# Kernel tuning notes

Measured on AMD Instinct MI355X. Metric: run time of the kernel, lower is better.

The kernel has to match this reference:

```python
import jax, jax.numpy as jnp
import numpy as np

B, N, D, H, DM = 4, 1024, 1024, 16, 4096
DH = D // H
SCALE = DH ** -0.5
EPS = 1e-5


def layer_norm(x, g, b):
    mu = jnp.mean(x, axis=-1, keepdims=True)
    var = jnp.mean((x - mu) ** 2, axis=-1, keepdims=True)
    return (x - mu) * jax.lax.rsqrt(var + EPS) * g + b


def mha(q_in, k_in, v_in, Wq, bq, Wk, bk, Wv, bv, Wp, bp):
    # weights stored (in, out); torch Linear equivalent y = x @ W + b
    q = (q_in @ Wq + bq).reshape(B, -1, H, DH).transpose(0, 2, 1, 3)  # (B,H,Nq,DH)
    k = (k_in @ Wk + bk).reshape(B, -1, H, DH).transpose(0, 2, 1, 3)
    v = (v_in @ Wv + bv).reshape(B, -1, H, DH).transpose(0, 2, 1, 3)
    attn = jax.nn.softmax(jnp.einsum('bhqd,bhkd->bhqk', q, k) * SCALE, axis=-1)
    x = jnp.einsum('bhqk,bhkd->bhqd', attn, v).transpose(0, 2, 1, 3).reshape(B, -1, D)
    return x @ Wp + bp


def setup_inputs() -> dict:
    key = jax.random.key(0)
    ks = jax.random.split(key, 32)
    s = 0.02
    inp = {
        'tokens_enc': jax.random.normal(ks[0], (B, N, D), jnp.float32),
        'tokens_dec': jax.random.normal(ks[1], (B, N, D), jnp.float32),
        'PE_enc': jax.random.normal(ks[2], (B, N, D), jnp.float32),
        'PE_dec': jax.random.normal(ks[3], (B, N, D), jnp.float32),
    }
    names = ['sa_Wq', 'sa_Wk', 'sa_Wv', 'sa_Wp', 'ca_Wq', 'ca_Wk', 'ca_Wv', 'ca_Wp']
    for i, n in enumerate(names):
        inp[n] = jax.random.normal(ks[4 + i], (D, D), jnp.float32) * s
        inp[n.replace('W', 'b')] = jnp.zeros((D,), jnp.float32)
    inp['mlp_W1'] = jax.random.normal(ks[12], (D, DM), jnp.float32) * s
    inp['mlp_b1'] = jnp.zeros((DM,), jnp.float32)
    inp['mlp_W2'] = jax.random.normal(ks[13], (DM, D), jnp.float32) * s
    inp['mlp_b2'] = jnp.zeros((D,), jnp.float32)
    for i in (1, 2, 3):
        inp[f'ln{i}_g'] = jnp.ones((D,), jnp.float32)
        inp[f'ln{i}_b'] = jnp.zeros((D,), jnp.float32)
    return inp


def reference(tokens_enc, tokens_dec, PE_enc, PE_dec,
              sa_Wq, sa_bq, sa_Wk, sa_bk, sa_Wv, sa_bv, sa_Wp, sa_bp,
              ca_Wq, ca_bq, ca_Wk, ca_bk, ca_Wv, ca_bv, ca_Wp, ca_bp,
              mlp_W1, mlp_b1, mlp_W2, mlp_b2,
              ln1_g, ln1_b, ln2_g, ln2_b, ln3_g, ln3_b):
    # SA (pre-norm): q=k=ln(x)+PE_dec, v=ln(x)
    x2 = layer_norm(tokens_dec, ln1_g, ln1_b)
    qk = x2 + PE_dec
    tokens_dec = tokens_dec + mha(qk, qk, x2, sa_Wq, sa_bq, sa_Wk, sa_bk, sa_Wv, sa_bv, sa_Wp, sa_bp)
    # CA: q=ln(x)+PE_dec, k=enc+PE_enc, v=enc
    x2 = layer_norm(tokens_dec, ln2_g, ln2_b)
    tokens_dec = tokens_dec + mha(x2 + PE_dec, tokens_enc + PE_enc, tokens_enc,
                                  ca_Wq, ca_bq, ca_Wk, ca_bk, ca_Wv, ca_bv, ca_Wp, ca_bp)
    # FFD
    x2 = layer_norm(tokens_dec, ln3_g, ln3_b)
    h = jax.nn.gelu(x2 @ mlp_W1 + mlp_b1, approximate=False)
    return tokens_dec + (h @ mlp_W2 + mlp_b2)
```

## Files before the change

kernel.cpp:

```cpp
#include <hip/hip_runtime.h>
#include <hip/hip_bf16.h>
#include <math.h>

#define B_ 4
#define N_ 1024
#define D_ 1024
#define H_ 16
#define DH_ 64
#define DM_ 4096
#define NT_ (B_*N_)
#define EPS_ 1e-5f
#define SCALE_ 0.125f
#define CEXP_ 0.1803368801111244f

typedef unsigned short u16;
typedef short s16x8 __attribute__((ext_vector_type(8)));
typedef __bf16 y16x8 __attribute__((ext_vector_type(8)));
typedef float f32x4 __attribute__((ext_vector_type(4)));
typedef float f32x16 __attribute__((ext_vector_type(16)));

#define ZERO16 (f32x16){0.f,0.f,0.f,0.f,0.f,0.f,0.f,0.f,0.f,0.f,0.f,0.f,0.f,0.f,0.f,0.f}

__device__ __forceinline__ u16 f2bs(float f) {
  unsigned int u = __builtin_bit_cast(unsigned int, f);
  u += 0x7fffu + ((u >> 16) & 1u);
  return (u16)(u >> 16);
}

static __device__ __forceinline__ f32x4 MFMA(y16x8 a, y16x8 b, f32x4 c) {
  return __builtin_amdgcn_mfma_f32_16x16x32_bf16(a, b, c, 0, 0, 0);
}
static __device__ __forceinline__ f32x16 MFMA32(y16x8 a, y16x8 b, f32x16 c) {
  return __builtin_amdgcn_mfma_f32_32x32x16_bf16(a, b, c, 0, 0, 0);
}

static __device__ __forceinline__ unsigned cvtpk(float a, float b) {
  unsigned r;
  asm("v_cvt_pk_bf16_f32 %0, %1, %2" : "=v"(r) : "v"(a), "v"(b));
  return r;
}

static __device__ __forceinline__ void async16(void* lds, const void* g) {
  __builtin_amdgcn_global_load_lds(
      (const __attribute__((address_space(1))) unsigned int*)g,
      (__attribute__((address_space(3))) unsigned int*)lds, 16, 0, 0);
}

__global__ __launch_bounds__(256) void k_wtrans8(
    const float* __restrict__ s0, const float* __restrict__ s1,
    const float* __restrict__ s2, const float* __restrict__ s3,
    const float* __restrict__ s4, const float* __restrict__ s5,
    const float* __restrict__ s6, const float* __restrict__ s7,
    u16* __restrict__ dst) {
  const float* W = blockIdx.z == 0 ? s0 : blockIdx.z == 1 ? s1 : blockIdx.z == 2 ? s2
                 : blockIdx.z == 3 ? s3 : blockIdx.z == 4 ? s4 : blockIdx.z == 5 ? s5
                 : blockIdx.z == 6 ? s6 : s7;
  u16* Wt = dst + (size_t)blockIdx.z * D_ * D_;
  __shared__ u16 tile[32][33];
  int n0 = blockIdx.x * 32, k0 = blockIdx.y * 32;
  int tx = threadIdx.x & 31, ty = threadIdx.x >> 5;
#pragma unroll
  for (int i = 0; i < 4; ++i) {
    int k = k0 + ty + i * 8;
    tile[ty + i * 8][tx] = f2bs(W[(size_t)k * D_ + n0 + tx]);
  }
  __syncthreads();
#pragma unroll
  for (int i = 0; i < 4; ++i) {
    int n = n0 + ty + i * 8;
    Wt[(size_t)n * D_ + k0 + tx] = tile[tx][ty + i * 8];
  }
}

__global__ __launch_bounds__(256) void k_wtrans(const float* __restrict__ W,
                                                u16* __restrict__ Wt,
                                                int K, int Ncols) {
  __shared__ u16 tile[32][33];
  int n0 = blockIdx.x * 32, k0 = blockIdx.y * 32;
  int tx = threadIdx.x & 31, ty = threadIdx.x >> 5;
#pragma unroll
  for (int i = 0; i < 4; ++i) {
    int k = k0 + ty + i * 8;
    tile[ty + i * 8][tx] = f2bs(W[(size_t)k * Ncols + n0 + tx]);
  }
  __syncthreads();
#pragma unroll
  for (int i = 0; i < 4; ++i) {
    int n = n0 + ty + i * 8;
    Wt[(size_t)n * K + k0 + tx] = tile[tx][ty + i * 8];
  }
}

__global__ __launch_bounds__(256) void k_encprep(const float* __restrict__ enc,
                                                 const float* __restrict__ pe,
                                                 u16* __restrict__ encpe,
                                                 u16* __restrict__ encv) {
  int i = blockIdx.x * 256 + threadIdx.x;
  float4 e = ((const float4*)enc)[i];
  float4 p = ((const float4*)pe)[i];
  union { u16 u[4]; uint2 v; } a, b;
  a.u[0] = f2bs(e.x + p.x); a.u[1] = f2bs(e.y + p.y);
  a.u[2] = f2bs(e.z + p.z); a.u[3] = f2bs(e.w + p.w);
  b.u[0] = f2bs(e.x); b.u[1] = f2bs(e.y); b.u[2] = f2bs(e.z); b.u[3] = f2bs(e.w);
  ((uint2*)encpe)[i] = a.v;
  ((uint2*)encv)[i] = b.v;
}

__global__ __launch_bounds__(256) void k_ln(const float* __restrict__ x,
                                            const float* __restrict__ g,
                                            const float* __restrict__ bta,
                                            const float* __restrict__ pe,
                                            u16* __restrict__ x2o,
                                            u16* __restrict__ qko) {
  int row = blockIdx.x;
  int t = threadIdx.x;
  float4 v = ((const float4*)(x + (size_t)row * D_))[t];
  float s = v.x + v.y + v.z + v.w;
#pragma unroll
  for (int o = 1; o < 64; o <<= 1) s += __shfl_xor(s, o, 64);
  __shared__ float red[8];
  if ((t & 63) == 0) red[t >> 6] = s;
  __syncthreads();
  float mean = (red[0] + red[1] + red[2] + red[3]) * (1.0f / D_);
  float dx = v.x - mean, dy = v.y - mean, dz = v.z - mean, dw = v.w - mean;
  float s2 = dx * dx + dy * dy + dz * dz + dw * dw;
#pragma unroll
  for (int o = 1; o < 64; o <<= 1) s2 += __shfl_xor(s2, o, 64);
  if ((t & 63) == 0) red[4 + (t >> 6)] = s2;
  __syncthreads();
  float var = (red[4] + red[5] + red[6] + red[7]) * (1.0f / D_);
  float rstd = rsqrtf(var + EPS_);
  float4 gv = ((const float4*)g)[t];
  float4 bv = ((const float4*)bta)[t];
  float y0 = dx * rstd * gv.x + bv.x;
  float y1 = dy * rstd * gv.y + bv.y;
  float y2 = dz * rstd * gv.z + bv.z;
  float y3 = dw * rstd * gv.w + bv.w;
  union { u16 u[4]; uint2 v2; } o1;
  o1.u[0] = f2bs(y0); o1.u[1] = f2bs(y1); o1.u[2] = f2bs(y2); o1.u[3] = f2bs(y3);
  ((uint2*)(x2o + (size_t)row * D_))[t] = o1.v2;
  if (pe) {
    float4 pv = ((const float4*)(pe + (size_t)row * D_))[t];
    union { u16 u[4]; uint2 v2; } o2;
    o2.u[0] = f2bs(y0 + pv.x); o2.u[1] = f2bs(y1 + pv.y);
    o2.u[2] = f2bs(y2 + pv.z); o2.u[3] = f2bs(y3 + pv.w);
    ((uint2*)(qko + (size_t)row * D_))[t] = o2.v2;
  }
}

template <int EPI, int BM>
__global__ __launch_bounds__(512) void k_gemm(const u16* __restrict__ A,
                                              const u16* __restrict__ Bt,
                                              const float* __restrict__ bias,
                                              const float* __restrict__ res,
                                              float* __restrict__ outf,
                                              u16* __restrict__ outb,
                                              int M, int Nn, int K, int ldo) {
  constexpr int BN = 128, BK = 64;
  constexpr int FM = BM / 32;
  __shared__ __align__(128) char smem[2][(BM + BN) * BK * 2];
  const int t = threadIdx.x;
  const int wave = t >> 6, lane = t & 63, lg = lane >> 4, lc = lane & 15;
  const int nwg = gridDim.x * gridDim.y;
  const int bid = blockIdx.y * gridDim.x + blockIdx.x;
  const int lb = (bid & 7) * (nwg >> 3) + (bid >> 3);
  const int bx = lb % gridDim.x, by = lb / gridDim.x;
  const int m0 = by * BM, n0 = bx * BN;
  const int wm = (wave >> 2) * (BM / 2), wn = (wave & 3) * 32;
  f32x4 acc[FM][2];
#pragma unroll
  for (int i = 0; i < FM; ++i)
#pragma unroll
    for (int j = 0; j < 2; ++j) acc[i][j] = (f32x4){0.f, 0.f, 0.f, 0.f};
  const char* Ag = (const char*)(A + (size_t)m0 * K);
  const char* Bg = (const char*)(Bt + (size_t)n0 * K);
  const int sr = t >> 3, sp = t & 7;

  auto stage = [&](int bufi, int kt) {
    char* sA = smem[bufi];
    char* sB = smem[bufi] + BM * BK * 2;
#pragma unroll
    for (int rr = 0; rr < BM / 64; ++rr) {
      int row = rr * 64 + sr;
      int c = sp ^ (row & 7);
      async16(sA + (size_t)row * 128 + sp * 16,
              Ag + ((size_t)row * K + kt + c * 8) * 2);
    }
#pragma unroll
    for (int rr = 0; rr < 2; ++rr) {
      int row = rr * 64 + sr;
      int c = sp ^ (row & 7);
      async16(sB + (size_t)row * 128 + sp * 16,
              Bg + ((size_t)row * K + kt + c * 8) * 2);
    }
  };
  auto compute = [&](int bufi) {
    const char* sA = smem[bufi];
    const char* sB = smem[bufi] + BM * BK * 2;
#pragma unroll
    for (int ks = 0; ks < 2; ++ks) {
      y16x8 af[FM], bfr[2];
#pragma unroll
      for (int fm = 0; fm < FM; ++fm) {
        int R = wm + fm * 16 + lc;
        int pc = (ks * 4 + lg) ^ (R & 7);
        af[fm] = *(const y16x8*)(sA + (size_t)R * 128 + pc * 16);
      }
#pragma unroll
      for (int fn = 0; fn < 2; ++fn) {
        int R = wn + fn * 16 + lc;
        int pc = (ks * 4 + lg) ^ (R & 7);
        bfr[fn] = *(const y16x8*)(sB + (size_t)R * 128 + pc * 16);
      }
#pragma unroll
      for (int fm = 0; fm < FM; ++fm)
#pragma unroll
        for (int fn = 0; fn < 2; ++fn)
          acc[fm][fn] = MFMA(af[fm], bfr[fn], acc[fm][fn]);
    }
  };

  stage(0, 0);
  __syncthreads();
  int cur = 0;
  for (int kt = BK; kt < K; kt += BK) {
    stage(cur ^ 1, kt);
    compute(cur);
    __syncthreads();
    cur ^= 1;
  }
  compute(cur);

#pragma unroll
  for (int fm = 0; fm < FM; ++fm)
#pragma unroll
    for (int fn = 0; fn < 2; ++fn)
#pragma unroll
      for (int j = 0; j < 4; ++j) {
        int row = m0 + wm + fm * 16 + lg * 4 + j;
        int col = n0 + wn + fn * 16 + lc;
        float vv = acc[fm][fn][j] + bias[col];
        size_t idx = (size_t)row * ldo + col;
        if constexpr (EPI == 0) {
          outb[idx] = f2bs(vv);
        } else if constexpr (EPI == 1) {
          outf[idx] = vv + res[idx];
        } else {
          float gx = 0.5f * vv * (1.0f + erff(vv * 0.70710678118f));
          outb[idx] = f2bs(gx);
        }
      }
}

__global__ __launch_bounds__(512) void k_gemmG(
    const u16* __restrict__ A0, const u16* __restrict__ A1,
    const u16* __restrict__ A2, const u16* __restrict__ A3,
    const u16* __restrict__ A4, const u16* __restrict__ W0,
    const u16* __restrict__ W1, const u16* __restrict__ W2,
    const u16* __restrict__ W3, const u16* __restrict__ W4,
    const float* __restrict__ b0, const float* __restrict__ b1,
    const float* __restrict__ b2, const float* __restrict__ b3,
    const float* __restrict__ b4, u16* __restrict__ qk1,
    u16* __restrict__ vt1, u16* __restrict__ qk2, u16* __restrict__ vt2) {
  constexpr int BM = 128, BN = 128, BK = 64, K = D_;
  __shared__ __align__(128) char smem[2][(BM + BN) * BK * 2];
  const int z = blockIdx.z;
  const u16* A = z == 0 ? A0 : z == 1 ? A1 : z == 2 ? A2 : z == 3 ? A3 : A4;
  const u16* Bt = z == 0 ? W0 : z == 1 ? W1 : z == 2 ? W2 : z == 3 ? W3 : W4;
  const float* bias = z == 0 ? b0 : z == 1 ? b1 : z == 2 ? b2 : z == 3 ? b3 : b4;
  const int t = threadIdx.x;
  const int wave = t >> 6, lane = t & 63, lg = lane >> 4, lc = lane & 15;
  const int nwg = gridDim.x * gridDim.y;
  const int bid = blockIdx.y * gridDim.x + blockIdx.x;
  const int lb = (bid & 7) * (nwg >> 3) + (bid >> 3);
  const int bx = lb % gridDim.x, by = lb / gridDim.x;
  const int m0 = by * BM, n0 = bx * BN;
  const int wm = (wave >> 2) * 64, wn = (wave & 3) * 32;
  f32x4 acc[4][2];
#pragma unroll
  for (int i = 0; i < 4; ++i)
#pragma unroll
    for (int j = 0; j < 2; ++j) acc[i][j] = (f32x4){0.f, 0.f, 0.f, 0.f};
  const char* Ag = (const char*)(A + (size_t)m0 * K);
  const char* Bg = (const char*)(Bt + (size_t)n0 * K);
  const int sr = t >> 3, sp = t & 7;

  auto stage = [&](int bufi, int kt) {
    char* sA = smem[bufi];
    char* sB = smem[bufi] + BM * BK * 2;
#pragma unroll
    for (int rr = 0; rr < 2; ++rr) {
      int row = rr * 64 + sr;
      int c = sp ^ (row & 7);
      async16(sA + (size_t)row * 128 + sp * 16,
              Ag + ((size_t)row * K + kt + c * 8) * 2);
      async16(sB + (size_t)row * 128 + sp * 16,
              Bg + ((size_t)row * K + kt + c * 8) * 2);
    }
  };
  auto compute = [&](int bufi) {
    const char* sA = smem[bufi];
    const char* sB = smem[bufi] + BM * BK * 2;
#pragma unroll
    for (int ks = 0; ks < 2; ++ks) {
      y16x8 af[4], bfr[2];
#pragma unroll
      for (int fm = 0; fm < 4; ++fm) {
        int R = wm + fm * 16 + lc;
        int pc = (ks * 4 + lg) ^ (R & 7);
        af[fm] = *(const y16x8*)(sA + (size_t)R * 128 + pc * 16);
      }
#pragma unroll
      for (int fn = 0; fn < 2; ++fn) {
        int R = wn + fn * 16 + lc;
        int pc = (ks * 4 + lg) ^ (R & 7);
        bfr[fn] = *(const y16x8*)(sB + (size_t)R * 128 + pc * 16);
      }
#pragma unroll
      for (int fm = 0; fm < 4; ++fm)
#pragma unroll
        for (int fn = 0; fn < 2; ++fn)
          acc[fm][fn] = MFMA(af[fm], bfr[fn], acc[fm][fn]);
    }
  };

  stage(0, 0);
  __syncthreads();
  int cur = 0;
  for (int kt = BK; kt < K; kt += BK) {
    stage(cur ^ 1, kt);
    compute(cur);
    __syncthreads();
    cur ^= 1;
  }
  compute(cur);

  const bool isV = (z == 2) || (z == 4);
  if (!isV) {
    u16* outqk = (z == 3) ? qk2 : qk1;
    const int coff = (z == 1 || z == 3) ? D_ : 0;
#pragma unroll
    for (int fm = 0; fm < 4; ++fm)
#pragma unroll
      for (int fn = 0; fn < 2; ++fn)
#pragma unroll
        for (int j = 0; j < 4; ++j) {
          int row = m0 + wm + fm * 16 + lg * 4 + j;
          int col = n0 + wn + fn * 16 + lc;
          outqk[(size_t)row * (2 * D_) + coff + col] =
              f2bs(acc[fm][fn][j] + bias[col]);
        }
  } else {
    u16* outvt = (z == 2) ? vt1 : vt2;
#pragma unroll
    for (int fm = 0; fm < 4; ++fm)
#pragma unroll
      for (int fn = 0; fn < 2; ++fn) {
        int row0 = m0 + wm + fm * 16 + lg * 4;
        int col = n0 + wn + fn * 16 + lc;
        int bb = row0 >> 10, nn = row0 & (N_ - 1);
        int h = col >> 6, dh = col & 63;
        float bcol = bias[col];
        union { u16 u[4]; uint2 v; } pk;
#pragma unroll
        for (int j = 0; j < 4; ++j) pk.u[j] = f2bs(acc[fm][fn][j] + bcol);
        *(uint2*)&outvt[(((size_t)bb * H_ + h) * DH_ + dh) * N_ + nn] = pk.v;
      }
  }
}

__global__ __launch_bounds__(256) void k_attn(const u16* __restrict__ q, int qs,
                                              const u16* __restrict__ k, int ks2,
                                              const u16* __restrict__ vt,
                                              u16* __restrict__ out) {
  __shared__ __align__(16) u16 Kl[64][64];
  __shared__ __align__(16) u16 Vl[64][64];
  __shared__ __align__(16) u16 Ol[4][32][72];
  const int lb = blockIdx.x;
  const int bh = (lb & 7) | ((lb >> 6) << 3);
  const int qb = (lb >> 3) & 7;
  const int b = bh >> 4, h = bh & 15;
  const int t = threadIdx.x, wave = t >> 6, lane = t & 63;
  const int ql = lane & 31, hi = lane >> 5;
  const int q0 = qb * 128 + wave * 32;
  const u16* qp = q + ((size_t)b * N_ + q0) * qs + h * DH_;
  const u16* kp = k + (size_t)b * N_ * ks2 + h * DH_;
  const u16* vp = vt + ((size_t)bh * DH_) * N_;

  y16x8 aq[4];
#pragma unroll
  for (int s = 0; s < 4; ++s)
    aq[s] = *(const y16x8*)(qp + (size_t)ql * qs + s * 16 + hi * 8);

  f32x16 o0 = ZERO16, o1 = ZERO16;
  float m_r = -1e30f, l_r = 0.f;

  const int srow0 = t >> 3, sc = t & 7;
  s16x8 kreg[2], vreg[2];
#pragma unroll
  for (int rr = 0; rr < 2; ++rr) {
    int row = rr * 32 + srow0;
    kreg[rr] = *(const s16x8*)(kp + (size_t)row * ks2 + sc * 8);
    vreg[rr] = *(const s16x8*)(vp + (size_t)row * N_ + sc * 8);
  }

  for (int kt = 0; kt < N_; kt += 64) {
    __syncthreads();
#pragma unroll
    for (int rr = 0; rr < 2; ++rr) {
      int row = rr * 32 + srow0;
      int pc2 = sc ^ (row & 7);
      *(s16x8*)&Kl[row][pc2 * 8] = kreg[rr];
      *(s16x8*)&Vl[row][pc2 * 8] = vreg[rr];
    }
    __syncthreads();
    if (kt + 64 < N_) {
#pragma unroll
      for (int rr = 0; rr < 2; ++rr) {
        int row = rr * 32 + srow0;
        kreg[rr] = *(const s16x8*)(kp + (size_t)(kt + 64 + row) * ks2 + sc * 8);
        vreg[rr] = *(const s16x8*)(vp + (size_t)row * N_ + kt + 64 + sc * 8);
      }
    }

    f32x16 st0 = ZERO16, st1 = ZERO16;
    __builtin_amdgcn_s_setprio(1);
#pragma unroll
    for (int s = 0; s < 4; ++s) {
      int pc0 = ((s * 2 + hi) ^ (ql & 7)) * 8;
      y16x8 ak0 = *(const y16x8*)&Kl[ql][pc0];
      y16x8 ak1 = *(const y16x8*)&Kl[32 + ql][pc0];
      st0 = MFMA32(ak0, aq[s], st0);
      st1 = MFMA32(ak1, aq[s], st1);
    }
    __builtin_amdgcn_s_setprio(0);

    float mx = st0[0];
#pragma unroll
    for (int r = 1; r < 16; ++r) mx = fmaxf(mx, st0[r]);
#pragma unroll
    for (int r = 0; r < 16; ++r) mx = fmaxf(mx, st1[r]);
    mx = fmaxf(mx, __shfl_xor(mx, 32, 64));
    if (!__all(mx - m_r <= 32.f)) {
      float mn = fmaxf(m_r, mx);
      float corr = exp2f((m_r - mn) * CEXP_);
      l_r *= corr;
      o0 = o0 * corr;
      o1 = o1 * corr;
      m_r = mn;
    }
    float ps = 0.f;
#pragma unroll
    for (int r = 0; r < 16; ++r) {
      float e = exp2f((st0[r] - m_r) * CEXP_); st0[r] = e; ps += e;
    }
#pragma unroll
    for (int r = 0; r < 16; ++r) {
      float e = exp2f((st1[r] - m_r) * CEXP_); st1[r] = e; ps += e;
    }
    ps += __shfl_xor(ps, 32, 64);
    l_r += ps;

    __builtin_amdgcn_s_setprio(1);
#pragma unroll
    for (int ks = 0; ks < 4; ++ks) {
      unsigned A0, A1, B0, B1;
      if (ks < 2) {
        const int il = ks * 8;
        A0 = cvtpk(st0[il + 0], st0[il + 1]);
        A1 = cvtpk(st0[il + 2], st0[il + 3]);
        B0 = cvtpk(st0[il + 4], st0[il + 5]);
        B1 = cvtpk(st0[il + 6], st0[il + 7]);
      } else {
        const int il = (ks - 2) * 8;
        A0 = cvtpk(st1[il + 0], st1[il + 1]);
        A1 = cvtpk(st1[il + 2], st1[il + 3]);
        B0 = cvtpk(st1[il + 4], st1[il + 5]);
        B1 = cvtpk(st1[il + 6], st1[il + 7]);
      }
      asm("v_permlane32_swap_b32 %0, %1" : "+v"(A0), "+v"(B0));
      asm("v_permlane32_swap_b32 %0, %1" : "+v"(A1), "+v"(B1));
      union { unsigned w[4]; y16x8 v; } fr;
      fr.w[0] = A0; fr.w[1] = A1; fr.w[2] = B0; fr.w[3] = B1;
      int pc = ((ks * 2 + hi) ^ (ql & 7)) * 8;
      y16x8 bv0 = *(const y16x8*)&Vl[ql][pc];
      y16x8 bv1 = *(const y16x8*)&Vl[32 + ql][pc];
      o0 = MFMA32(bv0, fr.v, o0);
      o1 = MFMA32(bv1, fr.v, o1);
    }
    __builtin_amdgcn_s_setprio(0);
  }

  float rl = 1.f / l_r;
#pragma unroll
  for (int rq = 0; rq < 4; ++rq)
#pragma unroll
    for (int e = 0; e < 4; e += 2) {
      *(unsigned*)&Ol[wave][ql][8 * rq + 4 * hi + e] =
          cvtpk(o0[rq * 4 + e] * rl, o0[rq * 4 + e + 1] * rl);
      *(unsigned*)&Ol[wave][ql][32 + 8 * rq + 4 * hi + e] =
          cvtpk(o1[rq * 4 + e] * rl, o1[rq * 4 + e + 1] * rl);
    }
#pragma unroll
  for (int pp = 0; pp < 4; ++pp) {
    int row = pp * 8 + (lane >> 3);
    s16x8 vv = *(const s16x8*)&Ol[wave][row][(lane & 7) * 8];
    *(s16x8*)(out + ((size_t)b * N_ + q0 + row) * D_ + h * DH_ + (lane & 7) * 8) = vv;
  }
}

extern "C" void kernel_launch(void* const* d_in, const int* in_sizes, int n_in,
                              void* d_out, int out_size, void* d_ws, size_t ws_size,
                              hipStream_t stream) {
  const float* tokens_enc = (const float*)d_in[0];
  const float* tokens_dec = (const float*)d_in[1];
  const float* PE_enc = (const float*)d_in[2];
  const float* PE_dec = (const float*)d_in[3];
  const float* sa_Wq = (const float*)d_in[4];  const float* sa_bq = (const float*)d_in[5];
  const float* sa_Wk = (const float*)d_in[6];  const float* sa_bk = (const float*)d_in[7];
  const float* sa_Wv = (const float*)d_in[8];  const float* sa_bv = (const float*)d_in[9];
  const float* sa_Wp = (const float*)d_in[10]; const float* sa_bp = (const float*)d_in[11];
  const float* ca_Wq = (const float*)d_in[12]; const float* ca_bq = (const float*)d_in[13];
  const float* ca_Wk = (const float*)d_in[14]; const float* ca_bk = (const float*)d_in[15];
  const float* ca_Wv = (const float*)d_in[16]; const float* ca_bv = (const float*)d_in[17];
  const float* ca_Wp = (const float*)d_in[18]; const float* ca_bp = (const float*)d_in[19];
  const float* mlp_W1 = (const float*)d_in[20]; const float* mlp_b1 = (const float*)d_in[21];
  const float* mlp_W2 = (const float*)d_in[22]; const float* mlp_b2 = (const float*)d_in[23];
  const float* ln1_g = (const float*)d_in[24]; const float* ln1_b = (const float*)d_in[25];
  const float* ln2_g = (const float*)d_in[26]; const float* ln2_b = (const float*)d_in[27];
  const float* ln3_g = (const float*)d_in[28]; const float* ln3_b = (const float*)d_in[29];

  char* wsp = (char*)d_ws;
  size_t off = 0;
  auto alloc = [&](size_t bytes) -> char* {
    char* p = wsp + off;
    off += (bytes + 255) & ~(size_t)255;
    return p;
  };
  u16* w8   = (u16*)alloc((size_t)8 * D_ * D_ * 2);
  u16* w1T  = (u16*)alloc((size_t)DM_ * D_ * 2);
  u16* w2T  = (u16*)alloc((size_t)D_ * DM_ * 2);
  u16* encpe = (u16*)alloc((size_t)NT_ * D_ * 2);
  u16* encv  = (u16*)alloc((size_t)NT_ * D_ * 2);
  u16* x2b = (u16*)alloc((size_t)NT_ * D_ * 2);
  u16* qkb = (u16*)alloc((size_t)NT_ * D_ * 2);
  u16* qkm = (u16*)alloc((size_t)NT_ * 2 * D_ * 2);
  u16* qkm2 = (u16*)alloc((size_t)NT_ * 2 * D_ * 2);
  u16* vtb = (u16*)alloc((size_t)NT_ * D_ * 2);
  u16* vtb2 = (u16*)alloc((size_t)NT_ * D_ * 2);
  u16* attb = (u16*)alloc((size_t)NT_ * D_ * 2);
  float* dec1 = (float*)alloc((size_t)NT_ * D_ * 4);
  float* dec2 = (float*)alloc((size_t)NT_ * D_ * 4);
  u16* hb = (u16*)alloc((size_t)NT_ * DM_ * 2);

  const size_t DD = (size_t)D_ * D_;
  u16* wqT  = w8;
  u16* wkT  = w8 + 1 * DD;
  u16* wvT  = w8 + 2 * DD;
  u16* wpT  = w8 + 3 * DD;
  u16* cwqT = w8 + 4 * DD;
  u16* cwkT = w8 + 5 * DD;
  u16* cwvT = w8 + 6 * DD;
  u16* cwpT = w8 + 7 * DD;

  k_wtrans8<<<dim3(32, 32, 8), 256, 0, stream>>>(sa_Wq, sa_Wk, sa_Wv, sa_Wp,
                                                 ca_Wq, ca_Wk, ca_Wv, ca_Wp, w8);
  k_wtrans<<<dim3(128, 32), 256, 0, stream>>>(mlp_W1, w1T, D_, DM_);
  k_wtrans<<<dim3(32, 128), 256, 0, stream>>>(mlp_W2, w2T, DM_, D_);
  k_encprep<<<dim3(NT_ * D_ / 1024), 256, 0, stream>>>(tokens_enc, PE_enc, encpe, encv);

  k_ln<<<dim3(NT_), 256, 0, stream>>>(tokens_dec, ln1_g, ln1_b, PE_dec, x2b, qkb);
  k_gemmG<<<dim3(8, 32, 5), 512, 0, stream>>>(
      qkb, qkb, x2b, encpe, encv, wqT, wkT, wvT, cwkT, cwvT,
      sa_bq, sa_bk, sa_bv, ca_bk, ca_bv, qkm, vtb, qkm2, vtb2);
  k_attn<<<dim3(512), 256, 0, stream>>>(qkm, 2 * D_, qkm + D_, 2 * D_, vtb, attb);
  k_gemm<1, 64><<<dim3(8, 64), 512, 0, stream>>>(attb, wpT, sa_bp, tokens_dec,
                                                 dec1, nullptr, NT_, D_, D_, D_);

  k_ln<<<dim3(NT_), 256, 0, stream>>>(dec1, ln2_g, ln2_b, PE_dec, x2b, qkb);
  k_gemm<0, 64><<<dim3(8, 64), 512, 0, stream>>>(qkb, cwqT, ca_bq, nullptr,
                                                 nullptr, qkm2, NT_, D_, D_, 2 * D_);
  k_attn<<<dim3(512), 256, 0, stream>>>(qkm2, 2 * D_, qkm2 + D_, 2 * D_, vtb2, attb);
  k_gemm<1, 64><<<dim3(8, 64), 512, 0, stream>>>(attb, cwpT, ca_bp, dec1,
                                                 dec2, nullptr, NT_, D_, D_, D_);

  k_ln<<<dim3(NT_), 256, 0, stream>>>(dec2, ln3_g, ln3_b, nullptr, x2b, nullptr);
  k_gemm<2, 128><<<dim3(32, 32), 512, 0, stream>>>(x2b, w1T, mlp_b1, nullptr,
                                                   nullptr, hb, NT_, DM_, D_, DM_);
  k_gemm<1, 64><<<dim3(8, 64), 512, 0, stream>>>(hb, w2T, mlp_b2, dec2,
                                                 (float*)d_out, nullptr, NT_, D_, DM_, D_);
}
```

Measured before the change: 336.7 us.

## Merge prep kernels, double attention KV tile, shrink MLP1 GEMM tile

Folds the four preprocessing launches (weight transposes and encoder prep) into one kernel that dispatches on block index, which cuts launch overhead. The attention kernel now stages 128 keys per iteration instead of 64 and processes them in two 64-key sub-steps. That halves the barriers and global-load rounds per key, at the cost of more LDS and registers. The first MLP GEMM switches from a 128 to a 64 tile template with twice the grid, trading per-block reuse for more parallelism.

```diff
diff --git a/kernel.cpp b/kernel.cpp
--- a/kernel.cpp
+++ b/kernel.cpp
@@ -46,64 +46,62 @@
       (__attribute__((address_space(3))) unsigned int*)lds, 16, 0, 0);
 }
 
-__global__ __launch_bounds__(256) void k_wtrans8(
+__global__ __launch_bounds__(256) void k_prep(
     const float* __restrict__ s0, const float* __restrict__ s1,
     const float* __restrict__ s2, const float* __restrict__ s3,
     const float* __restrict__ s4, const float* __restrict__ s5,
     const float* __restrict__ s6, const float* __restrict__ s7,
-    u16* __restrict__ dst) {
-  const float* W = blockIdx.z == 0 ? s0 : blockIdx.z == 1 ? s1 : blockIdx.z == 2 ? s2
-                 : blockIdx.z == 3 ? s3 : blockIdx.z == 4 ? s4 : blockIdx.z == 5 ? s5
-                 : blockIdx.z == 6 ? s6 : s7;
-  u16* Wt = dst + (size_t)blockIdx.z * D_ * D_;
+    u16* __restrict__ w8, const float* __restrict__ mW1,
+    u16* __restrict__ w1T, const float* __restrict__ mW2,
+    u16* __restrict__ w2T, const float* __restrict__ enc,
+    const float* __restrict__ pe, u16* __restrict__ encpe,
+    u16* __restrict__ encv) {
   __shared__ u16 tile[32][33];
-  int n0 = blockIdx.x * 32, k0 = blockIdx.y * 32;
-  int tx = threadIdx.x & 31, ty = threadIdx.x >> 5;
-#pragma unroll
-  for (int i = 0; i < 4; ++i) {
-    int k = k0 + ty + i * 8;
-    tile[ty + i * 8][tx] = f2bs(W[(size_t)k * D_ + n0 + tx]);
-  }
-  __syncthreads();
-#pragma unroll
-  for (int i = 0; i < 4; ++i) {
-    int n = n0 + ty + i * 8;
-    Wt[(size_t)n * D_ + k0 + tx] = tile[tx][ty + i * 8];
-  }
-}
-
-__global__ __launch_bounds__(256) void k_wtrans(const float* __restrict__ W,
-                                                u16* __restrict__ Wt,
-                                                int K, int Ncols) {
-  __shared__ u16 tile[32][33];
-  int n0 = blockIdx.x * 32, k0 = blockIdx.y * 32;
-  int tx = threadIdx.x & 31, ty = threadIdx.x >> 5;
-#pragma unroll
-  for (int i = 0; i < 4; ++i) {
-    int k = k0 + ty + i * 8;
-    tile[ty + i * 8][tx] = f2bs(W[(size_t)k * Ncols + n0 + tx]);
-  }
-  __syncthreads();
-#pragma unroll
-  for (int i = 0; i < 4; ++i) {
-    int n = n0 + ty + i * 8;
-    Wt[(size_t)n * K + k0 + tx] = tile[tx][ty + i * 8];
-  }
-}
-
-__global__ __launch_bounds__(256) void k_encprep(const float* __restrict__ enc,
-                                                 const float* __restrict__ pe,
-                                                 u16* __restrict__ encpe,
-                                                 u16* __restrict__ encv) {
-  int i = blockIdx.x * 256 + threadIdx.x;
-  float4 e = ((const float4*)enc)[i];
-  float4 p = ((const float4*)pe)[i];
-  union { u16 u[4]; uint2 v; } a, b;
-  a.u[0] = f2bs(e.x + p.x); a.u[1] = f2bs(e.y + p.y);
-  a.u[2] = f2bs(e.z + p.z); a.u[3] = f2bs(e.w + p.w);
-  b.u[0] = f2bs(e.x); b.u[1] = f2bs(e.y); b.u[2] = f2bs(e.z); b.u[3] = f2bs(e.w);
-  ((uint2*)encpe)[i] = a.v;
-  ((uint2*)encv)[i] = b.v;
+  const int gid = blockIdx.x;
+  const int t = threadIdx.x;
+  if (gid < 16384) {
+    const float* W;
+    u16* Wt;
+    int K, Ncols, n0, k0;
+    if (gid < 8192) {
+      int z = gid >> 10, rem = gid & 1023;
+      W = z == 0 ? s0 : z == 1 ? s1 : z == 2 ? s2 : z == 3 ? s3
+        : z == 4 ? s4 : z == 5 ? s5 : z == 6 ? s6 : s7;
+      Wt = w8 + (size_t)z * D_ * D_;
+      K = D_; Ncols = D_;
+      n0 = (rem & 31) * 32; k0 = (rem >> 5) * 32;
+    } else if (gid < 12288) {
+      int rem = gid - 8192;
+      W = mW1; Wt = w1T; K = D_; Ncols = DM_;
+      n0 = (rem & 127) * 32; k0 = (rem >> 7) * 32;
+    } else {
+      int rem = gid - 12288;
+      W = mW2; Wt = w2T; K = DM_; Ncols = D_;
+      n0 = (rem & 31) * 32; k0 = (rem >> 5) * 32;
+    }
+    int tx = t & 31, ty = t >> 5;
+#pragma unroll
+    for (int i = 0; i < 4; ++i) {
+      int k = k0 + ty + i * 8;
+      tile[ty + i * 8][tx] = f2bs(W[(size_t)k * Ncols + n0 + tx]);
+    }
+    __syncthreads();
+#pragma unroll
+    for (int i = 0; i < 4; ++i) {
+      int n = n0 + ty + i * 8;
+      Wt[(size_t)n * K + k0 + tx] = tile[tx][ty + i * 8];
+    }
+  } else {
+    int i = (gid - 16384) * 256 + t;
+    float4 e = ((const float4*)enc)[i];
+    float4 p = ((const float4*)pe)[i];
+    union { u16 u[4]; uint2 v; } a, b;
+    a.u[0] = f2bs(e.x + p.x); a.u[1] = f2bs(e.y + p.y);
+    a.u[2] = f2bs(e.z + p.z); a.u[3] = f2bs(e.w + p.w);
+    b.u[0] = f2bs(e.x); b.u[1] = f2bs(e.y); b.u[2] = f2bs(e.z); b.u[3] = f2bs(e.w);
+    ((uint2*)encpe)[i] = a.v;
+    ((uint2*)encv)[i] = b.v;
+  }
 }
 
 __global__ __launch_bounds__(256) void k_ln(const float* __restrict__ x,
@@ -373,8 +371,8 @@
                                               const u16* __restrict__ k, int ks2,
                                               const u16* __restrict__ vt,
                                               u16* __restrict__ out) {
-  __shared__ __align__(16) u16 Kl[64][64];
-  __shared__ __align__(16) u16 Vl[64][64];
+  __shared__ __align__(16) u16 Kl[128][64];
+  __shared__ __align__(16) u16 Vl[64][128];
   __shared__ __align__(16) u16 Ol[4][32][72];
   const int lb = blockIdx.x;
   const int bh = (lb & 7) | ((lb >> 6) << 3);
@@ -395,100 +393,103 @@
   f32x16 o0 = ZERO16, o1 = ZERO16;
   float m_r = -1e30f, l_r = 0.f;
 
-  const int srow0 = t >> 3, sc = t & 7;
-  s16x8 kreg[2], vreg[2];
-#pragma unroll
-  for (int rr = 0; rr < 2; ++rr) {
-    int row = rr * 32 + srow0;
-    kreg[rr] = *(const s16x8*)(kp + (size_t)row * ks2 + sc * 8);
-    vreg[rr] = *(const s16x8*)(vp + (size_t)row * N_ + sc * 8);
-  }
-
-  for (int kt = 0; kt < N_; kt += 64) {
+  const int kr = t >> 3, kc = t & 7;
+  const int vr = t >> 4, vc = t & 15;
+  s16x8 kreg[4], vreg[4];
+#pragma unroll
+  for (int rr = 0; rr < 4; ++rr) {
+    kreg[rr] = *(const s16x8*)(kp + (size_t)(rr * 32 + kr) * ks2 + kc * 8);
+    vreg[rr] = *(const s16x8*)(vp + (size_t)(rr * 16 + vr) * N_ + vc * 8);
+  }
+
+  for (int kt = 0; kt < N_; kt += 128) {
     __syncthreads();
 #pragma unroll
-    for (int rr = 0; rr < 2; ++rr) {
-      int row = rr * 32 + srow0;
-      int pc2 = sc ^ (row & 7);
-      *(s16x8*)&Kl[row][pc2 * 8] = kreg[rr];
-      *(s16x8*)&Vl[row][pc2 * 8] = vreg[rr];
+    for (int rr = 0; rr < 4; ++rr) {
+      int krow = rr * 32 + kr;
+      *(s16x8*)&Kl[krow][(kc ^ (krow & 7)) * 8] = kreg[rr];
+      int vrow = rr * 16 + vr;
+      *(s16x8*)&Vl[vrow][(vc ^ (vrow & 15)) * 8] = vreg[rr];
     }
     __syncthreads();
-    if (kt + 64 < N_) {
-#pragma unroll
-      for (int rr = 0; rr < 2; ++rr) {
-        int row = rr * 32 + srow0;
-        kreg[rr] = *(const s16x8*)(kp + (size_t)(kt + 64 + row) * ks2 + sc * 8);
-        vreg[rr] = *(const s16x8*)(vp + (size_t)row * N_ + kt + 64 + sc * 8);
-      }
-    }
-
-    f32x16 st0 = ZERO16, st1 = ZERO16;
-    __builtin_amdgcn_s_setprio(1);
-#pragma unroll
-    for (int s = 0; s < 4; ++s) {
-      int pc0 = ((s * 2 + hi) ^ (ql & 7)) * 8;
-      y16x8 ak0 = *(const y16x8*)&Kl[ql][pc0];
-      y16x8 ak1 = *(const y16x8*)&Kl[32 + ql][pc0];
-      st0 = MFMA32(ak0, aq[s], st0);
-      st1 = MFMA32(ak1, aq[s], st1);
-    }
-    __builtin_amdgcn_s_setprio(0);
-
-    float mx = st0[0];
-#pragma unroll
-    for (int r = 1; r < 16; ++r) mx = fmaxf(mx, st0[r]);
-#pragma unroll
-    for (int r = 0; r < 16; ++r) mx = fmaxf(mx, st1[r]);
-    mx = fmaxf(mx, __shfl_xor(mx, 32, 64));
-    if (!__all(mx - m_r <= 32.f)) {
-      float mn = fmaxf(m_r, mx);
-      float corr = exp2f((m_r - mn) * CEXP_);
-      l_r *= corr;
-      o0 = o0 * corr;
-      o1 = o1 * corr;
-      m_r = mn;
-    }
-    float ps = 0.f;
-#pragma unroll
-    for (int r = 0; r < 16; ++r) {
-      float e = exp2f((st0[r] - m_r) * CEXP_); st0[r] = e; ps += e;
-    }
-#pragma unroll
-    for (int r = 0; r < 16; ++r) {
-      float e = exp2f((st1[r] - m_r) * CEXP_); st1[r] = e; ps += e;
-    }
-    ps += __shfl_xor(ps, 32, 64);
-    l_r += ps;
-
-    __builtin_amdgcn_s_setprio(1);
-#pragma unroll
-    for (int ks = 0; ks < 4; ++ks) {
-      unsigned A0, A1, B0, B1;
-      if (ks < 2) {
-        const int il = ks * 8;
-        A0 = cvtpk(st0[il + 0], st0[il + 1]);
-        A1 = cvtpk(st0[il + 2], st0[il + 3]);
-        B0 = cvtpk(st0[il + 4], st0[il + 5]);
-        B1 = cvtpk(st0[il + 6], st0[il + 7]);
-      } else {
-        const int il = (ks - 2) * 8;
-        A0 = cvtpk(st1[il + 0], st1[il + 1]);
-        A1 = cvtpk(st1[il + 2], st1[il + 3]);
-        B0 = cvtpk(st1[il + 4], st1[il + 5]);
-        B1 = cvtpk(st1[il + 6], st1[il + 7]);
-      }
-      asm("v_permlane32_swap_b32 %0, %1" : "+v"(A0), "+v"(B0));
-      asm("v_permlane32_swap_b32 %0, %1" : "+v"(A1), "+v"(B1));
-      union { unsigned w[4]; y16x8 v; } fr;
-      fr.w[0] = A0; fr.w[1] = A1; fr.w[2] = B0; fr.w[3] = B1;
-      int pc = ((ks * 2 + hi) ^ (ql & 7)) * 8;
-      y16x8 bv0 = *(const y16x8*)&Vl[ql][pc];
-      y16x8 bv1 = *(const y16x8*)&Vl[32 + ql][pc];
-      o0 = MFMA32(bv0, fr.v, o0);
-      o1 = MFMA32(bv1, fr.v, o1);
-    }
-    __builtin_amdgcn_s_setprio(0);
+    if (kt + 128 < N_) {
+#pragma unroll
+      for (int rr = 0; rr < 4; ++rr) {
+        kreg[rr] = *(const s16x8*)(kp + (size_t)(kt + 128 + rr * 32 + kr) * ks2 + kc * 8);
+        vreg[rr] = *(const s16x8*)(vp + (size_t)(rr * 16 + vr) * N_ + kt + 128 + vc * 8);
+      }
+    }
+
+#pragma unroll
+    for (int sub = 0; sub < 2; ++sub) {
+      f32x16 st0 = ZERO16, st1 = ZERO16;
+      __builtin_amdgcn_s_setprio(1);
+#pragma unroll
+      for (int s = 0; s < 4; ++s) {
+        int pc0 = ((s * 2 + hi) ^ (ql & 7)) * 8;
+        y16x8 ak0 = *(const y16x8*)&Kl[sub * 64 + ql][pc0];
+        y16x8 ak1 = *(const y16x8*)&Kl[sub * 64 + 32 + ql][pc0];
+        st0 = MFMA32(ak0, aq[s], st0);
+        st1 = MFMA32(ak1, aq[s], st1);
+      }
+      __builtin_amdgcn_s_setprio(0);
+
+      float mx = st0[0];
+#pragma unroll
+      for (int r = 1; r < 16; ++r) mx = fmaxf(mx, st0[r]);
+#pragma unroll
+      for (int r = 0; r < 16; ++r) mx = fmaxf(mx, st1[r]);
+      mx = fmaxf(mx, __shfl_xor(mx, 32, 64));
+      if (!__all(mx - m_r <= 32.f)) {
+        float mn = fmaxf(m_r, mx);
+        float corr = exp2f((m_r - mn) * CEXP_);
+        l_r *= corr;
+        o0 = o0 * corr;
+        o1 = o1 * corr;
+        m_r = mn;
+      }
+      float ps = 0.f;
+#pragma unroll
+      for (int r = 0; r < 16; ++r) {
+        float e = exp2f((st0[r] - m_r) * CEXP_); st0[r] = e; ps += e;
+      }
+#pragma unroll
+      for (int r = 0; r < 16; ++r) {
+        float e = exp2f((st1[r] - m_r) * CEXP_); st1[r] = e; ps += e;
+      }
+      ps += __shfl_xor(ps, 32, 64);
+      l_r += ps;
+
+      __builtin_amdgcn_s_setprio(1);
+#pragma unroll
+      for (int ks = 0; ks < 4; ++ks) {
+        unsigned A0, A1, B0, B1;
+        if (ks < 2) {
+          const int il = ks * 8;
+          A0 = cvtpk(st0[il + 0], st0[il + 1]);
+          A1 = cvtpk(st0[il + 2], st0[il + 3]);
+          B0 = cvtpk(st0[il + 4], st0[il + 5]);
+          B1 = cvtpk(st0[il + 6], st0[il + 7]);
+        } else {
+          const int il = (ks - 2) * 8;
+          A0 = cvtpk(st1[il + 0], st1[il + 1]);
+          A1 = cvtpk(st1[il + 2], st1[il + 3]);
+          B0 = cvtpk(st1[il + 4], st1[il + 5]);
+          B1 = cvtpk(st1[il + 6], st1[il + 7]);
+        }
+        asm("v_permlane32_swap_b32 %0, %1" : "+v"(A0), "+v"(B0));
+        asm("v_permlane32_swap_b32 %0, %1" : "+v"(A1), "+v"(B1));
+        union { unsigned w[4]; y16x8 v; } fr;
+        fr.w[0] = A0; fr.w[1] = A1; fr.w[2] = B0; fr.w[3] = B1;
+        int ch0 = (sub * 8 + ks * 2 + hi) ^ (ql & 15);
+        int ch1 = (sub * 8 + ks * 2 + hi) ^ ((32 + ql) & 15);
+        y16x8 bv0 = *(const y16x8*)&Vl[ql][ch0 * 8];
+        y16x8 bv1 = *(const y16x8*)&Vl[32 + ql][ch1 * 8];
+        o0 = MFMA32(bv0, fr.v, o0);
+        o1 = MFMA32(bv1, fr.v, o1);
+      }
+      __builtin_amdgcn_s_setprio(0);
+    }
   }
 
   float rl = 1.f / l_r;
@@ -563,11 +564,10 @@
   u16* cwvT = w8 + 6 * DD;
   u16* cwpT = w8 + 7 * DD;
 
-  k_wtrans8<<<dim3(32, 32, 8), 256, 0, stream>>>(sa_Wq, sa_Wk, sa_Wv, sa_Wp,
-                                                 ca_Wq, ca_Wk, ca_Wv, ca_Wp, w8);
-  k_wtrans<<<dim3(128, 32), 256, 0, stream>>>(mlp_W1, w1T, D_, DM_);
-  k_wtrans<<<dim3(32, 128), 256, 0, stream>>>(mlp_W2, w2T, DM_, D_);
-  k_encprep<<<dim3(NT_ * D_ / 1024), 256, 0, stream>>>(tokens_enc, PE_enc, encpe, encv);
+  k_prep<<<dim3(20480), 256, 0, stream>>>(sa_Wq, sa_Wk, sa_Wv, sa_Wp,
+                                          ca_Wq, ca_Wk, ca_Wv, ca_Wp, w8,
+                                          mlp_W1, w1T, mlp_W2, w2T,
+                                          tokens_enc, PE_enc, encpe, encv);
 
   k_ln<<<dim3(NT_), 256, 0, stream>>>(tokens_dec, ln1_g, ln1_b, PE_dec, x2b, qkb);
   k_gemmG<<<dim3(8, 32, 5), 512, 0, stream>>>(
@@ -585,8 +585,8 @@
                                                  dec2, nullptr, NT_, D_, D_, D_);
 
   k_ln<<<dim3(NT_), 256, 0, stream>>>(dec2, ln3_g, ln3_b, nullptr, x2b, nullptr);
-  k_gemm<2, 128><<<dim3(32, 32), 512, 0, stream>>>(x2b, w1T, mlp_b1, nullptr,
-                                                   nullptr, hb, NT_, DM_, D_, DM_);
+  k_gemm<2, 64><<<dim3(32, 64), 512, 0, stream>>>(x2b, w1T, mlp_b1, nullptr,
+                                                  nullptr, hb, NT_, DM_, D_, DM_);
   k_gemm<1, 64><<<dim3(8, 64), 512, 0, stream>>>(hb, w2T, mlp_b2, dec2,
                                                  (float*)d_out, nullptr, NT_, D_, DM_, D_);
 }
```

Measured after the change: 335.3 us. Within noise of the previous version (-0.4%).
